# Optimization experiments

Hardware: AMD Instinct MI355X
Metric: run time of the kernel (lower is better)

Reference implementation:

```python
import jax, jax.numpy as jnp
import numpy as np

B, S, E, NH = 2, 2048, 1024, 8
DH = E // NH


def setup_inputs() -> dict:
    key = jax.random.key(0)
    ks = jax.random.split(key, 8)
    q = jax.random.normal(ks[0], (B, S, E), dtype=jnp.float32)
    k = jax.random.normal(ks[1], (B, S, E), dtype=jnp.float32)
    v = jax.random.normal(ks[2], (B, S, E), dtype=jnp.float32)
    # gate projections: Linear(3E -> NH)
    igate_w = jax.random.normal(ks[3], (NH, 3 * E), dtype=jnp.float32) * 0.02
    igate_b = jax.random.normal(ks[4], (NH,), dtype=jnp.float32) * 0.1
    fgate_w = jax.random.normal(ks[5], (NH, 3 * E), dtype=jnp.float32) * 0.02
    fgate_b = jnp.linspace(3.0, 6.0, NH, dtype=jnp.float32)  # bias_linspace_init_
    norm_weight = 1.0 + 0.01 * jax.random.normal(ks[6], (E,), dtype=jnp.float32)
    return {"q": q, "k": k, "v": v, "igate_w": igate_w, "igate_b": igate_b,
            "fgate_w": fgate_w, "fgate_b": fgate_b, "norm_weight": norm_weight}


def _mlstm_forward(q, k, v, igate_w, igate_b, fgate_w, fgate_b, norm_weight):
    eps = 1e-6
    gate_in = jnp.concatenate([q, k, v], axis=-1)            # (B,S,3E)
    i_pre = gate_in @ igate_w.T + igate_b                    # (B,S,NH)
    f_pre = gate_in @ fgate_w.T + fgate_b                    # (B,S,NH)
    i_pre = jnp.transpose(i_pre, (0, 2, 1))                  # (B,NH,S)
    f_pre = jnp.transpose(f_pre, (0, 2, 1))                  # (B,NH,S)

    qh = jnp.transpose(q.reshape(B, S, NH, DH), (0, 2, 1, 3))  # (B,NH,S,DH)
    kh = jnp.transpose(k.reshape(B, S, NH, DH), (0, 2, 1, 3))
    vh = jnp.transpose(v.reshape(B, S, NH, DH), (0, 2, 1, 3))

    # cumulative log forget gates; decay matrix D[i,j] = sum_{u=j+1..i} logsig(f_u) + i_pre[j]
    log_fg = jax.nn.log_sigmoid(f_pre)                       # (B,NH,S)
    cs = jnp.cumsum(log_fg, axis=-1)                         # (B,NH,S)
    diff = cs[:, :, :, None] - cs[:, :, None, :]             # (B,NH,S,S) = cs[i]-cs[j]
    causal = jnp.tril(jnp.ones((S, S), dtype=bool))
    log_fg_mat = jnp.where(causal, diff, -jnp.inf)
    log_D = log_fg_mat + i_pre[:, :, None, :]                # (B,NH,S,S)

    max_log_D = jnp.max(log_D, axis=-1, keepdims=True)       # rowwise stabilizer
    D = jnp.exp(log_D - max_log_D)

    qk = jnp.einsum("bhsd,bhtd->bhst", qh, kh / jnp.sqrt(jnp.float32(DH)))
    C = qk * D
    normalizer = jnp.maximum(jnp.abs(jnp.sum(C, axis=-1, keepdims=True)),
                             jnp.exp(-max_log_D))
    Cn = C / (normalizer + eps)
    h = jnp.einsum("bhst,bhtd->bhsd", Cn, vh)                # (B,NH,S,DH)

    # MultiHeadLayerNorm == group_norm(num_groups=NH): per-head, per-token over DH
    mu = jnp.mean(h, axis=-1, keepdims=True)
    var = jnp.var(h, axis=-1, keepdims=True)
    hn = (h - mu) / jnp.sqrt(var + 1e-5)
    hn = hn * norm_weight.reshape(NH, DH)[None, :, None, :]
    return jnp.transpose(hn, (0, 2, 1, 3)).reshape(B, S, E)


def reference(q, k, v, igate_w, igate_b, fgate_w, fgate_b, norm_weight):
    return _mlstm_forward(q, k, v, igate_w, igate_b, fgate_w, fgate_b, norm_weight)
```

## Files before the change

### kernel.cpp

```cpp
#include <hip/hip_runtime.h>
#include <hip/hip_bf16.h>
#include <math.h>

typedef __attribute__((ext_vector_type(8))) short bf16x8;
typedef __attribute__((ext_vector_type(16))) float f32x16;

namespace {
constexpr int kB = 2, kS = 2048, kE = 1024, kNH = 8, kDH = 128, kE3 = 3072;
constexpr float kLog2e = 1.4426950408889634f;
constexpr int kUnits = 27;
constexpr int kSplitPerBh = 20;
}

__device__ const int kOrder[kUnits] = {6,19,20,17,18,5,15,16,13,14,24,25,4,
                                       11,12,21,22,23,26,9,10,3,7,8,2,1,0};

__device__ __forceinline__ ushort f2bf(float x) {
  union { __hip_bfloat16 b; ushort u; } c; c.b = __float2bfloat16(x); return c.u;
}
__device__ __forceinline__ uint pk2(float a, float b) {
  return (uint)f2bf(a) | ((uint)f2bf(b) << 16);
}
__device__ __forceinline__ void gload16(const void* g, void* l) {
  __builtin_amdgcn_global_load_lds(
      (const __attribute__((address_space(1))) void*)g,
      (__attribute__((address_space(3))) void*)l, 16, 0, 0);
}
__device__ __forceinline__ f32x16 zero16() {
  f32x16 z;
#pragma unroll
  for (int i = 0; i < 16; ++i) z[i] = 0.f;
  return z;
}
union UB8 { uint4 u; bf16x8 f; };

__device__ __forceinline__ float butterfly64(float* acc, int lane) {
  int cur = 64;
#pragma unroll
  for (int lv = 0; lv < 6; ++lv) {
    const int bmask = 1 << lv;
    const int half = cur >> 1;
    const bool hi = (lane & bmask) != 0;
#pragma unroll
    for (int i = 0; i < 32; ++i) {
      if (i >= half) break;
      const float keep = hi ? acc[i + half] : acc[i];
      const float send = hi ? acc[i] : acc[i + half];
      acc[i] = keep + __shfl_xor(send, bmask);
    }
    cur = half;
  }
  return acc[0];
}

__global__ __launch_bounds__(256) void convkv_kernel(
    const float* __restrict__ k, const float* __restrict__ v,
    ushort* __restrict__ Kb, ushort* __restrict__ Vtb) {
  const int bh = blockIdx.y;
  const int b = bh >> 3, h = bh & 7;
  const int s0 = blockIdx.x * 32;
  const int tid = threadIdx.x;
  __shared__ ushort Vst[32 * 128];

  const int tl = tid >> 3;
  const int d0 = (tid & 7) * 16;
  const int s = s0 + tl;
  {
    const size_t base = ((size_t)b * kS + s) * kE + h * kDH + d0;
    const float4 k0 = *reinterpret_cast<const float4*>(k + base);
    const float4 k1 = *reinterpret_cast<const float4*>(k + base + 4);
    const float4 k2 = *reinterpret_cast<const float4*>(k + base + 8);
    const float4 k3 = *reinterpret_cast<const float4*>(k + base + 12);
    uint4 pa, pb;
    pa.x = pk2(k0.x, k0.y); pa.y = pk2(k0.z, k0.w);
    pa.z = pk2(k1.x, k1.y); pa.w = pk2(k1.z, k1.w);
    pb.x = pk2(k2.x, k2.y); pb.y = pk2(k2.z, k2.w);
    pb.z = pk2(k3.x, k3.y); pb.w = pk2(k3.z, k3.w);
    ushort* kd = Kb + ((size_t)bh * kS + s) * 128 + d0;
    *reinterpret_cast<uint4*>(kd) = pa;
    *reinterpret_cast<uint4*>(kd + 8) = pb;

    const float4 v0 = *reinterpret_cast<const float4*>(v + base);
    const float4 v1 = *reinterpret_cast<const float4*>(v + base + 4);
    const float4 v2 = *reinterpret_cast<const float4*>(v + base + 8);
    const float4 v3 = *reinterpret_cast<const float4*>(v + base + 12);
    uint4 va, vb4;
    va.x = pk2(v0.x, v0.y); va.y = pk2(v0.z, v0.w);
    va.z = pk2(v1.x, v1.y); va.w = pk2(v1.z, v1.w);
    vb4.x = pk2(v2.x, v2.y); vb4.y = pk2(v2.z, v2.w);
    vb4.z = pk2(v3.x, v3.y); vb4.w = pk2(v3.z, v3.w);
    const int c0 = d0 >> 3;
    char* row = reinterpret_cast<char*>(Vst) + tl * 256;
    *reinterpret_cast<uint4*>(row + (((c0 + 0) ^ (tl & 15)) << 4)) = va;
    *reinterpret_cast<uint4*>(row + (((c0 + 1) ^ (tl & 15)) << 4)) = vb4;
  }
  __syncthreads();

  {
    const int d = tid >> 1, half = tid & 1;
    const int cd = d >> 3;
    const int od = (d & 7) * 2;
    uint tmp[8];
#pragma unroll
    for (int p = 0; p < 8; ++p) {
      const int t = half * 16 + 2 * p;
      const ushort u0 = *reinterpret_cast<const ushort*>(
          reinterpret_cast<const char*>(Vst) + t * 256 + ((cd ^ (t & 15)) << 4) + od);
      const ushort u1 = *reinterpret_cast<const ushort*>(
          reinterpret_cast<const char*>(Vst) + (t + 1) * 256 + ((cd ^ ((t + 1) & 15)) << 4) + od);
      tmp[p] = (uint)u0 | ((uint)u1 << 16);
    }
    ushort* vd = Vtb + ((size_t)bh * kDH + d) * kS + s0 + half * 16;
    uint4 o0, o1;
    o0.x = tmp[0]; o0.y = tmp[1]; o0.z = tmp[2]; o0.w = tmp[3];
    o1.x = tmp[4]; o1.y = tmp[5]; o1.z = tmp[6]; o1.w = tmp[7];
    *reinterpret_cast<uint4*>(vd) = o0;
    *reinterpret_cast<uint4*>(vd + 8) = o1;
  }
}

__global__ __launch_bounds__(256) void gates_kernel(
    const float* __restrict__ q, const float* __restrict__ k, const float* __restrict__ v,
    const float* __restrict__ iw, const float* __restrict__ ib,
    const float* __restrict__ fw, const float* __restrict__ fb,
    float* __restrict__ i_pre, float* __restrict__ f_pre) {
  const int tid = threadIdx.x;
  const int w = tid >> 6, lane = tid & 63;
  const int tokbase = blockIdx.x * 4;
  float acc[64];
#pragma unroll
  for (int i = 0; i < 64; ++i) acc[i] = 0.f;

  for (int step = 0; step < 12; ++step) {
    const int e = w * 768 + step * 64 + lane;
    const int seg = e >> 10;
    const int eo = e & 1023;
    const float* __restrict__ src = (seg == 0) ? q : (seg == 1) ? k : v;
    float gv[4];
#pragma unroll
    for (int t = 0; t < 4; ++t)
      gv[t] = src[(size_t)(tokbase + t) * kE + eo];
    float wi[8], wf[8];
#pragma unroll
    for (int hh = 0; hh < 8; ++hh) {
      wi[hh] = iw[hh * kE3 + e];
      wf[hh] = fw[hh * kE3 + e];
    }
#pragma unroll
    for (int t = 0; t < 4; ++t) {
#pragma unroll
      for (int hh = 0; hh < 8; ++hh) {
        acc[t * 16 + hh]     += gv[t] * wi[hh];
        acc[t * 16 + 8 + hh] += gv[t] * wf[hh];
      }
    }
  }
  const float r = butterfly64(acc, lane);
  const int a = ((lane & 1) << 5) | ((lane & 2) << 3) | ((lane & 4) << 1) |
                ((lane & 8) >> 1) | ((lane & 16) >> 3) | ((lane & 32) >> 5);
  __shared__ float red[4][64];
  red[w][a] = r;
  __syncthreads();
  if (tid < 64) {
    const float val = red[0][tid] + red[1][tid] + red[2][tid] + red[3][tid];
    const int t = tid >> 4, gate = tid & 15, hh = gate & 7;
    const int token = tokbase + t;
    const int b = token >> 11, s = token & 2047;
    const size_t idx = ((size_t)(b * 8 + hh)) * kS + s;
    if (gate < 8) i_pre[idx] = val + ib[hh];
    else          f_pre[idx] = val + fb[hh];
  }
}

__global__ __launch_bounds__(256) void scan_kernel(
    const float* __restrict__ i_pre, const float* __restrict__ f_pre,
    float* __restrict__ wt_out, float* __restrict__ M2_out, float* __restrict__ nfl_out,
    float* __restrict__ Cg) {
  const int bh = blockIdx.x;
  const int tid = threadIdx.x;
  const int w = tid >> 6, lane = tid & 63;
  __shared__ float wsum[4], wmax[4];
  const float* __restrict__ fp = f_pre + (size_t)bh * kS;
  const float* __restrict__ ip = i_pre + (size_t)bh * kS;
  const int s0 = tid * 8;

  const float4 fa = *reinterpret_cast<const float4*>(fp + s0);
  const float4 fb4 = *reinterpret_cast<const float4*>(fp + s0 + 4);
  float lf[8];
  {
    const float fv[8] = {fa.x, fa.y, fa.z, fa.w, fb4.x, fb4.y, fb4.z, fb4.w};
#pragma unroll
    for (int j = 0; j < 8; ++j)
      lf[j] = fminf(fv[j], 0.f) - log1pf(expf(-fabsf(fv[j])));
  }
  float run = 0.f, pcs[8];
#pragma unroll
  for (int j = 0; j < 8; ++j) { run += lf[j]; pcs[j] = run; }
  float x = run;
#pragma unroll
  for (int d = 1; d < 64; d <<= 1) {
    const float t = __shfl_up(x, d);
    if (lane >= d) x += t;
  }
  if (lane == 63) wsum[w] = x;
  __syncthreads();
  float woff = 0.f;
#pragma unroll
  for (int i = 0; i < 4; ++i) if (i < w) woff += wsum[i];
  const float csbase = woff + x - run;
  float cs[8];
#pragma unroll
  for (int j = 0; j < 8; ++j) cs[j] = csbase + pcs[j];

  const float4 ia = *reinterpret_cast<const float4*>(ip + s0);
  const float4 ib4 = *reinterpret_cast<const float4*>(ip + s0 + 4);
  float av[8];
  {
    const float iv[8] = {ia.x, ia.y, ia.z, ia.w, ib4.x, ib4.y, ib4.z, ib4.w};
#pragma unroll
    for (int j = 0; j < 8; ++j) av[j] = iv[j] - cs[j];
  }
  float rmax = -1e30f, pm[8];
#pragma unroll
  for (int j = 0; j < 8; ++j) { rmax = fmaxf(rmax, av[j]); pm[j] = rmax; }

  float tm = rmax;
  tm = fmaxf(tm, __shfl_xor(tm, 1));
  tm = fmaxf(tm, __shfl_xor(tm, 2));
  tm = fmaxf(tm, __shfl_xor(tm, 4));
  if ((lane & 7) == 0) Cg[bh * 32 + (tid >> 3)] = tm * kLog2e;

  float4 wtlo, wthi;
  wtlo.x = exp2f((av[0] - tm) * kLog2e); wtlo.y = exp2f((av[1] - tm) * kLog2e);
  wtlo.z = exp2f((av[2] - tm) * kLog2e); wtlo.w = exp2f((av[3] - tm) * kLog2e);
  wthi.x = exp2f((av[4] - tm) * kLog2e); wthi.y = exp2f((av[5] - tm) * kLog2e);
  wthi.z = exp2f((av[6] - tm) * kLog2e); wthi.w = exp2f((av[7] - tm) * kLog2e);

  float mi = rmax;
#pragma unroll
  for (int d = 1; d < 64; d <<= 1) {
    const float t = __shfl_up(mi, d);
    if (lane >= d) mi = fmaxf(mi, t);
  }
  if (lane == 63) wmax[w] = mi;
  float mexcl = __shfl_up(mi, 1);
  if (lane == 0) mexcl = -1e30f;
  __syncthreads();
  float wmoff = -1e30f;
#pragma unroll
  for (int i = 0; i < 4; ++i) if (i < w) wmoff = fmaxf(wmoff, wmax[i]);
  const float mbase = fmaxf(wmoff, mexcl);

  float M[8];
#pragma unroll
  for (int j = 0; j < 8; ++j) M[j] = fmaxf(mbase, pm[j]);
  float4 m2lo, m2hi, nflo, nfhi;
  m2lo.x = M[0] * kLog2e; m2lo.y = M[1] * kLog2e; m2lo.z = M[2] * kLog2e; m2lo.w = M[3] * kLog2e;
  m2hi.x = M[4] * kLog2e; m2hi.y = M[5] * kLog2e; m2hi.z = M[6] * kLog2e; m2hi.w = M[7] * kLog2e;
  nflo.x = expf(-(cs[0] + M[0])); nflo.y = expf(-(cs[1] + M[1]));
  nflo.z = expf(-(cs[2] + M[2])); nflo.w = expf(-(cs[3] + M[3]));
  nfhi.x = expf(-(cs[4] + M[4])); nfhi.y = expf(-(cs[5] + M[5]));
  nfhi.z = expf(-(cs[6] + M[6])); nfhi.w = expf(-(cs[7] + M[7]));
  const size_t o = (size_t)bh * kS + s0;
  *reinterpret_cast<float4*>(wt_out + o) = wtlo;
  *reinterpret_cast<float4*>(wt_out + o + 4) = wthi;
  *reinterpret_cast<float4*>(M2_out + o) = m2lo;
  *reinterpret_cast<float4*>(M2_out + o + 4) = m2hi;
  *reinterpret_cast<float4*>(nfl_out + o) = nflo;
  *reinterpret_cast<float4*>(nfl_out + o + 4) = nfhi;
}

__global__ __launch_bounds__(256, 2) void attn_mfma_kernel(
    const float* __restrict__ qg, const ushort* __restrict__ Kb,
    const ushort* __restrict__ Vtb, const float* __restrict__ wt,
    const float* __restrict__ Cg, const float* __restrict__ M2,
    const float* __restrict__ nfl, const float* __restrict__ nw,
    float* __restrict__ out, float* __restrict__ ph, float* __restrict__ prs) {
  const int id = blockIdx.x;
  const int r8 = id & 7, qq = id >> 3;
  const int bh = r8 + 8 * (qq & 1);
  const int u = kOrder[qq >> 1];
  const int b = bh >> 3, h = bh & 7;
  int it, j0, j1, cid = -1;
  if (u <= 6) { it = u; const int T = 2 * it + 2; j0 = 0; j1 = T - 1; }
  else if (u <= 20) {
    const int s = u - 7; it = 7 + (s >> 1); const int ci = s & 1;
    const int T = 2 * it + 2;
    j0 = (T * ci) >> 1; j1 = ((T * (ci + 1)) >> 1) - 1;
    cid = bh * kSplitPerBh + (u - 7);
  } else {
    const int s = u - 21; it = 14 + (s >= 3 ? 1 : 0); const int ci = s - (s >= 3 ? 3 : 0);
    const int T = 2 * it + 2;
    j0 = (T * ci) / 3; j1 = (T * (ci + 1)) / 3 - 1;
    cid = bh * kSplitPerBh + (u - 7);
  }
  const int tid = threadIdx.x;
  const int w = tid >> 6, lane = tid & 63;
  const int l31 = lane & 31, hi = lane >> 5;
  const int row_w = it * 128 + w * 32;
  const int ig = row_w + l31;
  const size_t bhS = (size_t)bh * kS;

  __shared__ ushort Klds[2 * 64 * 128];
  __shared__ ushort Vlds[2 * 128 * 64];

  const char* __restrict__ KgBase = reinterpret_cast<const char*>(Kb + bhS * 128);
  const char* __restrict__ VgBase = reinterpret_cast<const char*>(Vtb + (size_t)bh * 128 * kS);
  const float* __restrict__ wtb = wt + bhS;

  bf16x8 qf[8];
  {
    const float scale = 0.08838834764831845f;
    const float* qrow = qg + ((size_t)b * kS + ig) * kE + h * kDH;
#pragma unroll
    for (int ks = 0; ks < 8; ++ks) {
      const int d0 = ks * 16 + hi * 8;
      const float4 lo = *reinterpret_cast<const float4*>(qrow + d0);
      const float4 hi4 = *reinterpret_cast<const float4*>(qrow + d0 + 4);
      UB8 f;
      f.u.x = pk2(lo.x * scale, lo.y * scale);
      f.u.y = pk2(lo.z * scale, lo.w * scale);
      f.u.z = pk2(hi4.x * scale, hi4.y * scale);
      f.u.w = pk2(hi4.z * scale, hi4.w * scale);
      qf[ks] = f.f;
    }
  }
  const float M2i = M2[bhS + ig];
  const float cgreg = Cg[bh * 32 + l31];

  int koffG[4], voffG[4];
#pragma unroll
  for (int i = 0; i < 4; ++i) {
    const int L = tid * 16 + i * 4096;
    { const int j = L >> 8, c = (L >> 4) & 15;
      koffG[i] = j * 256 + ((c ^ (j & 15)) << 4); }
    { const int d = L >> 7, c = (L >> 4) & 7;
      voffG[i] = d * 4096 + ((c ^ (d & 7)) << 4); }
  }
  auto stage = [&](int buf, int jt) {
    const char* Kg = KgBase + (size_t)jt * 16384;
    const char* Vg = VgBase + (size_t)jt * 128;
    char* kl = reinterpret_cast<char*>(Klds) + buf * 16384 + tid * 16;
    char* vl = reinterpret_cast<char*>(Vlds) + buf * 16384 + tid * 16;
#pragma unroll
    for (int i = 0; i < 4; ++i) gload16(Kg + koffG[i], kl + i * 4096);
#pragma unroll
    for (int i = 0; i < 4; ++i) gload16(Vg + voffG[i], vl + i * 4096);
  };

  f32x16 hacc[4];
#pragma unroll
  for (int dc = 0; dc < 4; ++dc) hacc[dc] = zero16();
  float rs = 0.f;

  float wtc0 = wtb[j0 * 64 + l31];
  float wtc1 = wtb[j0 * 64 + 32 + l31];
  stage(0, j0);
  __syncthreads();

  for (int jt = j0; jt <= j1; ++jt) {
    const int cur = (jt - j0) & 1;
    float wtn0, wtn1;
    if (jt < j1) {
      stage(cur ^ 1, jt + 1);
      wtn0 = wtb[(jt + 1) * 64 + l31];
      wtn1 = wtb[(jt + 1) * 64 + 32 + l31];
    }
    const int jlo = jt * 64;
    const bool v0 = (jlo <= row_w + 31);
    const bool v1 = (jlo + 32 <= row_w + 31);
    const bool fullmask = (jlo + 63 <= row_w);

    if (v0) {
      const float f = exp2f(__shfl(cgreg, jt) - M2i);
      const char* kb = reinterpret_cast<const char*>(Klds) + cur * 16384;
      const char* vb = reinterpret_cast<const char*>(Vlds) + cur * 16384;
      const int ksw = (l31 & 15) << 4;

      f32x16 sacc0 = zero16(), sacc1 = zero16();
#pragma unroll
      for (int ks = 0; ks < 8; ++ks) {
        const int colb = 32 * ks + 16 * hi;
        const bf16x8 kf0 = *reinterpret_cast<const bf16x8*>(
            kb + l31 * 256 + (colb ^ ksw));
        sacc0 = __builtin_amdgcn_mfma_f32_32x32x16_bf16(kf0, qf[ks], sacc0, 0, 0, 0);
        if (v1) {
          const bf16x8 kf1 = *reinterpret_cast<const bf16x8*>(
              kb + (32 + l31) * 256 + (colb ^ ksw));
          sacc1 = __builtin_amdgcn_mfma_f32_32x32x16_bf16(kf1, qf[ks], sacc1, 0, 0, 0);
        }
      }

      uint pkw[2][8];
#pragma unroll
      for (int jc = 0; jc < 2; ++jc) {
        if (jc == 1 && !v1) break;
        const f32x16 sa = jc ? sacc1 : sacc0;
        float p[16];
#pragma unroll
        for (int r = 0; r < 16; ++r) {
          const int c = (r & 3) + 8 * (r >> 2);
          const float wv = __shfl(jc ? wtc1 : wtc0, c + 4 * hi);
          float val = sa[r] * (wv * f);
          if (!fullmask) val = (jlo + jc * 32 + c + 4 * hi <= ig) ? val : 0.f;
          rs += val; p[r] = val;
        }
#pragma unroll
        for (int q2 = 0; q2 < 8; ++q2) pkw[jc][q2] = pk2(p[2 * q2], p[2 * q2 + 1]);
      }

#pragma unroll
      for (int ks = 0; ks < 4; ++ks) {
        const int jc = ks >> 1, ks2 = ks & 1;
        if (jc == 1 && !v1) break;
        UB8 pf;
        pf.u.x = pkw[jc][ks2 * 4 + 0]; pf.u.y = pkw[jc][ks2 * 4 + 1];
        pf.u.z = pkw[jc][ks2 * 4 + 2]; pf.u.w = pkw[jc][ks2 * 4 + 3];
        const int colb = 64 * jc + 32 * ks2 + 8 * hi;
#pragma unroll
        for (int dc = 0; dc < 4; ++dc) {
          const int d = dc * 32 + l31;
          const char* vrow = vb + d * 128;
          const int sw = (d & 7) << 4;
          const uint2 a = *reinterpret_cast<const uint2*>(vrow + (colb ^ sw));
          const uint2 c = *reinterpret_cast<const uint2*>(vrow + ((colb + 16) ^ sw));
          UB8 vf; vf.u.x = a.x; vf.u.y = a.y; vf.u.z = c.x; vf.u.w = c.y;
          hacc[dc] = __builtin_amdgcn_mfma_f32_32x32x16_bf16(pf.f, vf.f, hacc[dc], 0, 0, 0);
        }
      }
    }
    __syncthreads();
    if (jt < j1) { wtc0 = wtn0; wtc1 = wtn1; }
  }

  const float rs_tot = rs + __shfl_xor(rs, 32);

  if (cid >= 0) {
    float* pb = ph + (size_t)cid * 16384;
#pragma unroll
    for (int dc = 0; dc < 4; ++dc)
#pragma unroll
      for (int r = 0; r < 16; ++r) {
        const int il = w * 32 + (r & 3) + 8 * (r >> 2) + 4 * hi;
        pb[il * 128 + dc * 32 + l31] = hacc[dc][r];
      }
    if (hi == 0) prs[cid * 128 + w * 32 + l31] = rs_tot;
    return;
  }

  float nwv[4];
#pragma unroll
  for (int dc = 0; dc < 4; ++dc) nwv[dc] = nw[h * kDH + dc * 32 + l31];
#pragma unroll
  for (int r = 0; r < 16; ++r) {
    const int imap = (r & 3) + 8 * (r >> 2) + 4 * hi;
    const float rsum = __shfl(rs_tot, imap);
    const float nf = nfl[bhS + row_w + imap];
    const float inv = 1.f / (fmaxf(fabsf(rsum), nf) + 1e-6f);
    float hv[4];
    float s1 = 0.f, s2 = 0.f;
#pragma unroll
    for (int dc = 0; dc < 4; ++dc) {
      hv[dc] = hacc[dc][r] * inv;
      s1 += hv[dc]; s2 += hv[dc] * hv[dc];
    }
#pragma unroll
    for (int off = 1; off <= 16; off <<= 1) {
      s1 += __shfl_xor(s1, off);
      s2 += __shfl_xor(s2, off);
    }
    const float mu = s1 * (1.f / 128.f);
    const float var = s2 * (1.f / 128.f) - mu * mu;
    const float rstd = rsqrtf(var + 1e-5f);
    float* __restrict__ orow = out + ((size_t)b * kS + row_w + imap) * kE + h * kDH;
#pragma unroll
    for (int dc = 0; dc < 4; ++dc)
      orow[dc * 32 + l31] = (hv[dc] - mu) * rstd * nwv[dc];
  }
}

__global__ __launch_bounds__(256) void combine_kernel(
    const float* __restrict__ ph, const float* __restrict__ prs,
    const float* __restrict__ nfl, const float* __restrict__ nw,
    float* __restrict__ out) {
  const int blk = blockIdx.x;
  const int bh = blk / 9, ct = blk % 9;
  const int b = bh >> 3, h = bh & 7;
  const int it = 7 + ct;
  const int nc = (ct < 7) ? 2 : 3;
  const int cb0 = bh * kSplitPerBh + ((ct < 7) ? ct * 2 : 14 + (ct - 7) * 3);
  const int tid = threadIdx.x;
  __shared__ float sinv[128];
  if (tid < 128) {
    float rsum = 0.f;
    for (int c = 0; c < nc; ++c) rsum += prs[(cb0 + c) * 128 + tid];
    const float nf = nfl[(size_t)bh * kS + it * 128 + tid];
    sinv[tid] = 1.f / (fmaxf(fabsf(rsum), nf) + 1e-6f);
  }
  __syncthreads();
  for (int kk = 0; kk < 16; ++kk) {
    const int idx = kk * 256 + tid;
    const int row = idx >> 5, c4 = idx & 31;
    float ax = 0.f, ay = 0.f, az = 0.f, aw = 0.f;
    for (int c = 0; c < nc; ++c) {
      const float4 t = *reinterpret_cast<const float4*>(
          ph + (size_t)(cb0 + c) * 16384 + row * 128 + c4 * 4);
      ax += t.x; ay += t.y; az += t.z; aw += t.w;
    }
    const float inv = sinv[row];
    ax *= inv; ay *= inv; az *= inv; aw *= inv;
    float s1 = ax + ay + az + aw;
    float s2 = ax * ax + ay * ay + az * az + aw * aw;
#pragma unroll
    for (int off = 1; off <= 16; off <<= 1) {
      s1 += __shfl_xor(s1, off);
      s2 += __shfl_xor(s2, off);
    }
    const float mu = s1 * (1.f / 128.f);
    const float var = s2 * (1.f / 128.f) - mu * mu;
    const float rstd = rsqrtf(var + 1e-5f);
    const float4 nw4 = *reinterpret_cast<const float4*>(nw + h * kDH + c4 * 4);
    float4 o;
    o.x = (ax - mu) * rstd * nw4.x;
    o.y = (ay - mu) * rstd * nw4.y;
    o.z = (az - mu) * rstd * nw4.z;
    o.w = (aw - mu) * rstd * nw4.w;
    *reinterpret_cast<float4*>(
        out + ((size_t)b * kS + it * 128 + row) * kE + h * kDH + c4 * 4) = o;
  }
}

extern "C" void kernel_launch(void* const* d_in, const int* in_sizes, int n_in,
                              void* d_out, int out_size, void* d_ws, size_t ws_size,
                              hipStream_t stream) {
  const float* q  = (const float*)d_in[0];
  const float* k  = (const float*)d_in[1];
  const float* v  = (const float*)d_in[2];
  const float* iw = (const float*)d_in[3];
  const float* ib = (const float*)d_in[4];
  const float* fw = (const float*)d_in[5];
  const float* fb = (const float*)d_in[6];
  const float* nw = (const float*)d_in[7];
  float* out = (float*)d_out;

  char* ws = (char*)d_ws;
  const int BHS = kB * kNH * kS;
  float* i_pre = (float*)ws;
  float* f_pre = i_pre + BHS;
  float* wt    = i_pre + 2 * BHS;
  float* M2    = i_pre + 3 * BHS;
  float* nfl   = i_pre + 4 * BHS;
  float* Cg    = i_pre + 5 * BHS;
  ushort* Kb  = (ushort*)(ws + (size_t)(5 * BHS + 512) * 4);
  ushort* Vtb = Kb + (size_t)kB * kNH * kS * kDH;
  float* ph   = (float*)(Vtb + (size_t)kB * kNH * kS * kDH);
  float* prs  = ph + (size_t)320 * 128 * 128;

  convkv_kernel<<<dim3(kS / 32, kB * kNH), dim3(256), 0, stream>>>(k, v, Kb, Vtb);
  gates_kernel<<<dim3(kB * kS / 4), dim3(256), 0, stream>>>(q, k, v, iw, ib, fw, fb,
                                                            i_pre, f_pre);
  scan_kernel<<<dim3(kB * kNH), dim3(256), 0, stream>>>(i_pre, f_pre, wt, M2, nfl, Cg);
  attn_mfma_kernel<<<dim3(kUnits * kB * kNH), dim3(256), 0, stream>>>(
      q, Kb, Vtb, wt, Cg, M2, nfl, nw, out, ph, prs);
  combine_kernel<<<dim3(kB * kNH * 9), dim3(256), 0, stream>>>(ph, prs, nfl, nw, out);
}
```

Baseline: 123.0 us.

## Split attention key tiles across two wave groups and fuse prep kernels

The attention kernel now launches 512 threads, so two groups of four waves each handle one 32-key half of every 64-key tile. Their partial h accumulators and row sums are reduced through shared memory at the end. The aim is more waves per block, more latency hiding and less per-wave serial MFMA work, at the cost of an extra LDS reduction, more shared memory per block and register pressure from the launch bound of 4. Separately, the K/V conversion and gate projection kernels are merged into one launch with a branch on block index, saving one kernel launch.

```diff
diff --git a/kernel.cpp b/kernel.cpp
--- a/kernel.cpp
+++ b/kernel.cpp
@@ -53,122 +53,120 @@
   return acc[0];
 }
 
-__global__ __launch_bounds__(256) void convkv_kernel(
-    const float* __restrict__ k, const float* __restrict__ v,
-    ushort* __restrict__ Kb, ushort* __restrict__ Vtb) {
-  const int bh = blockIdx.y;
-  const int b = bh >> 3, h = bh & 7;
-  const int s0 = blockIdx.x * 32;
-  const int tid = threadIdx.x;
-  __shared__ ushort Vst[32 * 128];
-
-  const int tl = tid >> 3;
-  const int d0 = (tid & 7) * 16;
-  const int s = s0 + tl;
-  {
-    const size_t base = ((size_t)b * kS + s) * kE + h * kDH + d0;
-    const float4 k0 = *reinterpret_cast<const float4*>(k + base);
-    const float4 k1 = *reinterpret_cast<const float4*>(k + base + 4);
-    const float4 k2 = *reinterpret_cast<const float4*>(k + base + 8);
-    const float4 k3 = *reinterpret_cast<const float4*>(k + base + 12);
-    uint4 pa, pb;
-    pa.x = pk2(k0.x, k0.y); pa.y = pk2(k0.z, k0.w);
-    pa.z = pk2(k1.x, k1.y); pa.w = pk2(k1.z, k1.w);
-    pb.x = pk2(k2.x, k2.y); pb.y = pk2(k2.z, k2.w);
-    pb.z = pk2(k3.x, k3.y); pb.w = pk2(k3.z, k3.w);
-    ushort* kd = Kb + ((size_t)bh * kS + s) * 128 + d0;
-    *reinterpret_cast<uint4*>(kd) = pa;
-    *reinterpret_cast<uint4*>(kd + 8) = pb;
-
-    const float4 v0 = *reinterpret_cast<const float4*>(v + base);
-    const float4 v1 = *reinterpret_cast<const float4*>(v + base + 4);
-    const float4 v2 = *reinterpret_cast<const float4*>(v + base + 8);
-    const float4 v3 = *reinterpret_cast<const float4*>(v + base + 12);
-    uint4 va, vb4;
-    va.x = pk2(v0.x, v0.y); va.y = pk2(v0.z, v0.w);
-    va.z = pk2(v1.x, v1.y); va.w = pk2(v1.z, v1.w);
-    vb4.x = pk2(v2.x, v2.y); vb4.y = pk2(v2.z, v2.w);
-    vb4.z = pk2(v3.x, v3.y); vb4.w = pk2(v3.z, v3.w);
-    const int c0 = d0 >> 3;
-    char* row = reinterpret_cast<char*>(Vst) + tl * 256;
-    *reinterpret_cast<uint4*>(row + (((c0 + 0) ^ (tl & 15)) << 4)) = va;
-    *reinterpret_cast<uint4*>(row + (((c0 + 1) ^ (tl & 15)) << 4)) = vb4;
-  }
-  __syncthreads();
-
-  {
-    const int d = tid >> 1, half = tid & 1;
-    const int cd = d >> 3;
-    const int od = (d & 7) * 2;
-    uint tmp[8];
-#pragma unroll
-    for (int p = 0; p < 8; ++p) {
-      const int t = half * 16 + 2 * p;
-      const ushort u0 = *reinterpret_cast<const ushort*>(
-          reinterpret_cast<const char*>(Vst) + t * 256 + ((cd ^ (t & 15)) << 4) + od);
-      const ushort u1 = *reinterpret_cast<const ushort*>(
-          reinterpret_cast<const char*>(Vst) + (t + 1) * 256 + ((cd ^ ((t + 1) & 15)) << 4) + od);
-      tmp[p] = (uint)u0 | ((uint)u1 << 16);
-    }
-    ushort* vd = Vtb + ((size_t)bh * kDH + d) * kS + s0 + half * 16;
-    uint4 o0, o1;
-    o0.x = tmp[0]; o0.y = tmp[1]; o0.z = tmp[2]; o0.w = tmp[3];
-    o1.x = tmp[4]; o1.y = tmp[5]; o1.z = tmp[6]; o1.w = tmp[7];
-    *reinterpret_cast<uint4*>(vd) = o0;
-    *reinterpret_cast<uint4*>(vd + 8) = o1;
-  }
-}
-
-__global__ __launch_bounds__(256) void gates_kernel(
+__global__ __launch_bounds__(256) void prep_kernel(
     const float* __restrict__ q, const float* __restrict__ k, const float* __restrict__ v,
     const float* __restrict__ iw, const float* __restrict__ ib,
     const float* __restrict__ fw, const float* __restrict__ fb,
+    ushort* __restrict__ Kb, ushort* __restrict__ Vtb,
     float* __restrict__ i_pre, float* __restrict__ f_pre) {
+  const int bid = blockIdx.x;
   const int tid = threadIdx.x;
-  const int w = tid >> 6, lane = tid & 63;
-  const int tokbase = blockIdx.x * 4;
-  float acc[64];
-#pragma unroll
-  for (int i = 0; i < 64; ++i) acc[i] = 0.f;
-
-  for (int step = 0; step < 12; ++step) {
-    const int e = w * 768 + step * 64 + lane;
-    const int seg = e >> 10;
-    const int eo = e & 1023;
-    const float* __restrict__ src = (seg == 0) ? q : (seg == 1) ? k : v;
-    float gv[4];
-#pragma unroll
-    for (int t = 0; t < 4; ++t)
-      gv[t] = src[(size_t)(tokbase + t) * kE + eo];
-    float wi[8], wf[8];
-#pragma unroll
-    for (int hh = 0; hh < 8; ++hh) {
-      wi[hh] = iw[hh * kE3 + e];
-      wf[hh] = fw[hh * kE3 + e];
-    }
-#pragma unroll
-    for (int t = 0; t < 4; ++t) {
+  __shared__ ushort Vst[32 * 128];
+  __shared__ float red[4][64];
+
+  if (bid < 1024) {
+    const int bh = bid >> 6;
+    const int b = bh >> 3, h = bh & 7;
+    const int s0 = (bid & 63) * 32;
+    const int tl = tid >> 3;
+    const int d0 = (tid & 7) * 16;
+    const int s = s0 + tl;
+    {
+      const size_t base = ((size_t)b * kS + s) * kE + h * kDH + d0;
+      const float4 k0 = *reinterpret_cast<const float4*>(k + base);
+      const float4 k1 = *reinterpret_cast<const float4*>(k + base + 4);
+      const float4 k2 = *reinterpret_cast<const float4*>(k + base + 8);
+      const float4 k3 = *reinterpret_cast<const float4*>(k + base + 12);
+      uint4 pa, pb;
+      pa.x = pk2(k0.x, k0.y); pa.y = pk2(k0.z, k0.w);
+      pa.z = pk2(k1.x, k1.y); pa.w = pk2(k1.z, k1.w);
+      pb.x = pk2(k2.x, k2.y); pb.y = pk2(k2.z, k2.w);
+      pb.z = pk2(k3.x, k3.y); pb.w = pk2(k3.z, k3.w);
+      ushort* kd = Kb + ((size_t)bh * kS + s) * 128 + d0;
+      *reinterpret_cast<uint4*>(kd) = pa;
+      *reinterpret_cast<uint4*>(kd + 8) = pb;
+
+      const float4 v0 = *reinterpret_cast<const float4*>(v + base);
+      const float4 v1 = *reinterpret_cast<const float4*>(v + base + 4);
+      const float4 v2 = *reinterpret_cast<const float4*>(v + base + 8);
+      const float4 v3 = *reinterpret_cast<const float4*>(v + base + 12);
+      uint4 va, vb4;
+      va.x = pk2(v0.x, v0.y); va.y = pk2(v0.z, v0.w);
+      va.z = pk2(v1.x, v1.y); va.w = pk2(v1.z, v1.w);
+      vb4.x = pk2(v2.x, v2.y); vb4.y = pk2(v2.z, v2.w);
+      vb4.z = pk2(v3.x, v3.y); vb4.w = pk2(v3.z, v3.w);
+      const int c0 = d0 >> 3;
+      char* row = reinterpret_cast<char*>(Vst) + tl * 256;
+      *reinterpret_cast<uint4*>(row + (((c0 + 0) ^ (tl & 15)) << 4)) = va;
+      *reinterpret_cast<uint4*>(row + (((c0 + 1) ^ (tl & 15)) << 4)) = vb4;
+    }
+    __syncthreads();
+    {
+      const int d = tid >> 1, half = tid & 1;
+      const int cd = d >> 3;
+      const int od = (d & 7) * 2;
+      uint tmp[8];
+#pragma unroll
+      for (int p = 0; p < 8; ++p) {
+        const int t = half * 16 + 2 * p;
+        const ushort u0 = *reinterpret_cast<const ushort*>(
+            reinterpret_cast<const char*>(Vst) + t * 256 + ((cd ^ (t & 15)) << 4) + od);
+        const ushort u1 = *reinterpret_cast<const ushort*>(
+            reinterpret_cast<const char*>(Vst) + (t + 1) * 256 + ((cd ^ ((t + 1) & 15)) << 4) + od);
+        tmp[p] = (uint)u0 | ((uint)u1 << 16);
+      }
+      ushort* vd = Vtb + ((size_t)bh * kDH + d) * kS + s0 + half * 16;
+      uint4 o0, o1;
+      o0.x = tmp[0]; o0.y = tmp[1]; o0.z = tmp[2]; o0.w = tmp[3];
+      o1.x = tmp[4]; o1.y = tmp[5]; o1.z = tmp[6]; o1.w = tmp[7];
+      *reinterpret_cast<uint4*>(vd) = o0;
+      *reinterpret_cast<uint4*>(vd + 8) = o1;
+    }
+  } else {
+    const int w = tid >> 6, lane = tid & 63;
+    const int tokbase = (bid - 1024) * 4;
+    float acc[64];
+#pragma unroll
+    for (int i = 0; i < 64; ++i) acc[i] = 0.f;
+
+    for (int step = 0; step < 12; ++step) {
+      const int e = w * 768 + step * 64 + lane;
+      const int seg = e >> 10;
+      const int eo = e & 1023;
+      const float* __restrict__ src = (seg == 0) ? q : (seg == 1) ? k : v;
+      float gv[4];
+#pragma unroll
+      for (int t = 0; t < 4; ++t)
+        gv[t] = src[(size_t)(tokbase + t) * kE + eo];
+      float wi[8], wf[8];
 #pragma unroll
       for (int hh = 0; hh < 8; ++hh) {
-        acc[t * 16 + hh]     += gv[t] * wi[hh];
-        acc[t * 16 + 8 + hh] += gv[t] * wf[hh];
-      }
-    }
-  }
-  const float r = butterfly64(acc, lane);
-  const int a = ((lane & 1) << 5) | ((lane & 2) << 3) | ((lane & 4) << 1) |
-                ((lane & 8) >> 1) | ((lane & 16) >> 3) | ((lane & 32) >> 5);
-  __shared__ float red[4][64];
-  red[w][a] = r;
-  __syncthreads();
-  if (tid < 64) {
-    const float val = red[0][tid] + red[1][tid] + red[2][tid] + red[3][tid];
-    const int t = tid >> 4, gate = tid & 15, hh = gate & 7;
-    const int token = tokbase + t;
-    const int b = token >> 11, s = token & 2047;
-    const size_t idx = ((size_t)(b * 8 + hh)) * kS + s;
-    if (gate < 8) i_pre[idx] = val + ib[hh];
-    else          f_pre[idx] = val + fb[hh];
+        wi[hh] = iw[hh * kE3 + e];
+        wf[hh] = fw[hh * kE3 + e];
+      }
+#pragma unroll
+      for (int t = 0; t < 4; ++t) {
+#pragma unroll
+        for (int hh = 0; hh < 8; ++hh) {
+          acc[t * 16 + hh]     += gv[t] * wi[hh];
+          acc[t * 16 + 8 + hh] += gv[t] * wf[hh];
+        }
+      }
+    }
+    const float r = butterfly64(acc, lane);
+    const int a = ((lane & 1) << 5) | ((lane & 2) << 3) | ((lane & 4) << 1) |
+                  ((lane & 8) >> 1) | ((lane & 16) >> 3) | ((lane & 32) >> 5);
+    red[w][a] = r;
+    __syncthreads();
+    if (tid < 64) {
+      const float val = red[0][tid] + red[1][tid] + red[2][tid] + red[3][tid];
+      const int t = tid >> 4, gate = tid & 15, hh = gate & 7;
+      const int token = tokbase + t;
+      const int b = token >> 11, s = token & 2047;
+      const size_t idx = ((size_t)(b * 8 + hh)) * kS + s;
+      if (gate < 8) i_pre[idx] = val + ib[hh];
+      else          f_pre[idx] = val + fb[hh];
+    }
   }
 }
 
@@ -270,7 +268,7 @@
   *reinterpret_cast<float4*>(nfl_out + o + 4) = nfhi;
 }
 
-__global__ __launch_bounds__(256, 2) void attn_mfma_kernel(
+__global__ __launch_bounds__(512, 4) void attn_mfma_kernel(
     const float* __restrict__ qg, const ushort* __restrict__ Kb,
     const ushort* __restrict__ Vtb, const float* __restrict__ wt,
     const float* __restrict__ Cg, const float* __restrict__ M2,
@@ -296,13 +294,16 @@
   }
   const int tid = threadIdx.x;
   const int w = tid >> 6, lane = tid & 63;
+  const int wr = w & 3, jh = w >> 2;
   const int l31 = lane & 31, hi = lane >> 5;
-  const int row_w = it * 128 + w * 32;
+  const int row_w = it * 128 + wr * 32;
   const int ig = row_w + l31;
   const size_t bhS = (size_t)bh * kS;
 
-  __shared__ ushort Klds[2 * 64 * 128];
-  __shared__ ushort Vlds[2 * 128 * 64];
+  __shared__ char smem[66048];
+  ushort* Klds = reinterpret_cast<ushort*>(smem);
+  ushort* Vlds = reinterpret_cast<ushort*>(smem + 32768);
+  float* rsx2 = reinterpret_cast<float*>(smem + 65536);
 
   const char* __restrict__ KgBase = reinterpret_cast<const char*>(Kb + bhS * 128);
   const char* __restrict__ VgBase = reinterpret_cast<const char*>(Vtb + (size_t)bh * 128 * kS);
@@ -328,10 +329,10 @@
   const float M2i = M2[bhS + ig];
   const float cgreg = Cg[bh * 32 + l31];
 
-  int koffG[4], voffG[4];
-#pragma unroll
-  for (int i = 0; i < 4; ++i) {
-    const int L = tid * 16 + i * 4096;
+  int koffG[2], voffG[2];
+#pragma unroll
+  for (int i = 0; i < 2; ++i) {
+    const int L = tid * 16 + i * 8192;
     { const int j = L >> 8, c = (L >> 4) & 15;
       koffG[i] = j * 256 + ((c ^ (j & 15)) << 4); }
     { const int d = L >> 7, c = (L >> 4) & 7;
@@ -343,9 +344,9 @@
     char* kl = reinterpret_cast<char*>(Klds) + buf * 16384 + tid * 16;
     char* vl = reinterpret_cast<char*>(Vlds) + buf * 16384 + tid * 16;
 #pragma unroll
-    for (int i = 0; i < 4; ++i) gload16(Kg + koffG[i], kl + i * 4096);
-#pragma unroll
-    for (int i = 0; i < 4; ++i) gload16(Vg + voffG[i], vl + i * 4096);
+    for (int i = 0; i < 2; ++i) gload16(Kg + koffG[i], kl + i * 8192);
+#pragma unroll
+    for (int i = 0; i < 2; ++i) gload16(Vg + voffG[i], vl + i * 8192);
   };
 
   f32x16 hacc[4];
@@ -353,70 +354,57 @@
   for (int dc = 0; dc < 4; ++dc) hacc[dc] = zero16();
   float rs = 0.f;
 
-  float wtc0 = wtb[j0 * 64 + l31];
-  float wtc1 = wtb[j0 * 64 + 32 + l31];
+  float wtc = wtb[j0 * 64 + jh * 32 + l31];
   stage(0, j0);
   __syncthreads();
 
   for (int jt = j0; jt <= j1; ++jt) {
     const int cur = (jt - j0) & 1;
-    float wtn0, wtn1;
+    float wtn;
     if (jt < j1) {
       stage(cur ^ 1, jt + 1);
-      wtn0 = wtb[(jt + 1) * 64 + l31];
-      wtn1 = wtb[(jt + 1) * 64 + 32 + l31];
-    }
-    const int jlo = jt * 64;
-    const bool v0 = (jlo <= row_w + 31);
-    const bool v1 = (jlo + 32 <= row_w + 31);
-    const bool fullmask = (jlo + 63 <= row_w);
-
-    if (v0) {
+      wtn = wtb[(jt + 1) * 64 + jh * 32 + l31];
+    }
+    const int jlo = jt * 64 + jh * 32;
+    const bool valid = (jlo <= row_w + 31);
+    const bool fullmask = (jlo + 31 <= row_w);
+
+    if (valid) {
       const float f = exp2f(__shfl(cgreg, jt) - M2i);
       const char* kb = reinterpret_cast<const char*>(Klds) + cur * 16384;
       const char* vb = reinterpret_cast<const char*>(Vlds) + cur * 16384;
       const int ksw = (l31 & 15) << 4;
 
-      f32x16 sacc0 = zero16(), sacc1 = zero16();
+      f32x16 sacc = zero16();
 #pragma unroll
       for (int ks = 0; ks < 8; ++ks) {
         const int colb = 32 * ks + 16 * hi;
-        const bf16x8 kf0 = *reinterpret_cast<const bf16x8*>(
-            kb + l31 * 256 + (colb ^ ksw));
-        sacc0 = __builtin_amdgcn_mfma_f32_32x32x16_bf16(kf0, qf[ks], sacc0, 0, 0, 0);
-        if (v1) {
-          const bf16x8 kf1 = *reinterpret_cast<const bf16x8*>(
-              kb + (32 + l31) * 256 + (colb ^ ksw));
-          sacc1 = __builtin_amdgcn_mfma_f32_32x32x16_bf16(kf1, qf[ks], sacc1, 0, 0, 0);
-        }
-      }
-
-      uint pkw[2][8];
-#pragma unroll
-      for (int jc = 0; jc < 2; ++jc) {
-        if (jc == 1 && !v1) break;
-        const f32x16 sa = jc ? sacc1 : sacc0;
+        const bf16x8 kf = *reinterpret_cast<const bf16x8*>(
+            kb + (jh * 32 + l31) * 256 + (colb ^ ksw));
+        sacc = __builtin_amdgcn_mfma_f32_32x32x16_bf16(kf, qf[ks], sacc, 0, 0, 0);
+      }
+
+      uint pkw[8];
+      {
         float p[16];
 #pragma unroll
         for (int r = 0; r < 16; ++r) {
           const int c = (r & 3) + 8 * (r >> 2);
-          const float wv = __shfl(jc ? wtc1 : wtc0, c + 4 * hi);
-          float val = sa[r] * (wv * f);
-          if (!fullmask) val = (jlo + jc * 32 + c + 4 * hi <= ig) ? val : 0.f;
+          const float wv = __shfl(wtc, c + 4 * hi);
+          float val = sacc[r] * (wv * f);
+          if (!fullmask) val = (jlo + c + 4 * hi <= ig) ? val : 0.f;
           rs += val; p[r] = val;
         }
 #pragma unroll
-        for (int q2 = 0; q2 < 8; ++q2) pkw[jc][q2] = pk2(p[2 * q2], p[2 * q2 + 1]);
-      }
-
-#pragma unroll
-      for (int ks = 0; ks < 4; ++ks) {
-        const int jc = ks >> 1, ks2 = ks & 1;
-        if (jc == 1 && !v1) break;
+        for (int q2 = 0; q2 < 8; ++q2) pkw[q2] = pk2(p[2 * q2], p[2 * q2 + 1]);
+      }
+
+#pragma unroll
+      for (int ks2 = 0; ks2 < 2; ++ks2) {
         UB8 pf;
-        pf.u.x = pkw[jc][ks2 * 4 + 0]; pf.u.y = pkw[jc][ks2 * 4 + 1];
-        pf.u.z = pkw[jc][ks2 * 4 + 2]; pf.u.w = pkw[jc][ks2 * 4 + 3];
-        const int colb = 64 * jc + 32 * ks2 + 8 * hi;
+        pf.u.x = pkw[ks2 * 4 + 0]; pf.u.y = pkw[ks2 * 4 + 1];
+        pf.u.z = pkw[ks2 * 4 + 2]; pf.u.w = pkw[ks2 * 4 + 3];
+        const int colb = 64 * jh + 32 * ks2 + 8 * hi;
 #pragma unroll
         for (int dc = 0; dc < 4; ++dc) {
           const int d = dc * 32 + l31;
@@ -430,10 +418,28 @@
       }
     }
     __syncthreads();
-    if (jt < j1) { wtc0 = wtn0; wtc1 = wtn1; }
-  }
-
-  const float rs_tot = rs + __shfl_xor(rs, 32);
+    if (jt < j1) wtc = wtn;
+  }
+
+  const float rs_half = rs + __shfl_xor(rs, 32);
+  __syncthreads();
+  float* scratch = reinterpret_cast<float*>(smem);
+  if (jh == 1) {
+#pragma unroll
+    for (int dc = 0; dc < 4; ++dc)
+#pragma unroll
+      for (int r = 0; r < 16; ++r)
+        scratch[(dc * 16 + r) * 256 + wr * 64 + lane] = hacc[dc][r];
+    if (hi == 0) rsx2[wr * 32 + l31] = rs_half;
+  }
+  __syncthreads();
+  if (jh != 0) return;
+  const float rs_tot = rs_half + rsx2[wr * 32 + l31];
+#pragma unroll
+  for (int dc = 0; dc < 4; ++dc)
+#pragma unroll
+    for (int r = 0; r < 16; ++r)
+      hacc[dc][r] += scratch[(dc * 16 + r) * 256 + wr * 64 + lane];
 
   if (cid >= 0) {
     float* pb = ph + (size_t)cid * 16384;
@@ -441,10 +447,10 @@
     for (int dc = 0; dc < 4; ++dc)
 #pragma unroll
       for (int r = 0; r < 16; ++r) {
-        const int il = w * 32 + (r & 3) + 8 * (r >> 2) + 4 * hi;
+        const int il = wr * 32 + (r & 3) + 8 * (r >> 2) + 4 * hi;
         pb[il * 128 + dc * 32 + l31] = hacc[dc][r];
       }
-    if (hi == 0) prs[cid * 128 + w * 32 + l31] = rs_tot;
+    if (hi == 0) prs[cid * 128 + wr * 32 + l31] = rs_tot;
     return;
   }
 
@@ -556,11 +562,10 @@
   float* ph   = (float*)(Vtb + (size_t)kB * kNH * kS * kDH);
   float* prs  = ph + (size_t)320 * 128 * 128;
 
-  convkv_kernel<<<dim3(kS / 32, kB * kNH), dim3(256), 0, stream>>>(k, v, Kb, Vtb);
-  gates_kernel<<<dim3(kB * kS / 4), dim3(256), 0, stream>>>(q, k, v, iw, ib, fw, fb,
-                                                            i_pre, f_pre);
+  prep_kernel<<<dim3(2048), dim3(256), 0, stream>>>(q, k, v, iw, ib, fw, fb,
+                                                    Kb, Vtb, i_pre, f_pre);
   scan_kernel<<<dim3(kB * kNH), dim3(256), 0, stream>>>(i_pre, f_pre, wt, M2, nfl, Cg);
-  attn_mfma_kernel<<<dim3(kUnits * kB * kNH), dim3(256), 0, stream>>>(
+  attn_mfma_kernel<<<dim3(kUnits * kB * kNH), dim3(512), 0, stream>>>(
       q, Kb, Vtb, wt, Cg, M2, nfl, nw, out, ph, prs);
   combine_kernel<<<dim3(kB * kNH * 9), dim3(256), 0, stream>>>(ph, prs, nfl, nw, out);
 }
```

After: 157.5 us. 28.0% more time.
